# Performance work log

Measured on AMD Instinct MI355X. Metric: run time of the kernel, lower is better.

Reference implementation:

```python
import jax, jax.numpy as jnp
import numpy as np

N = 100000
E = 1600000
IN_DIM, HID, OUT = 256, 128, 64
K_HOPS = 5
ALPHA = 0.1
MLPA = 0.001


def setup_inputs() -> dict:
    key = jax.random.key(0)
    ks = jax.random.split(key, 20)
    s = 0.05
    inp = {
        "x": jax.random.normal(ks[0], (N, IN_DIM), jnp.float32),
        "edge_index": jax.random.randint(ks[1], (2, E), 0, N, jnp.int64),
        "edge_weight": jax.random.uniform(ks[2], (E,), jnp.float32),
        "A": jax.random.normal(ks[3], (N, 1), jnp.float32),
        # net1 MLP
        "m1_W1": jax.random.normal(ks[4], (IN_DIM, HID), jnp.float32) * s,
        "m1_b1": jnp.zeros((HID,), jnp.float32),
        "m1_W2": jax.random.normal(ks[5], (HID, OUT), jnp.float32) * s,
        "m1_b2": jnp.zeros((OUT,), jnp.float32),
        # net2 MLP
        "m2_W1": jax.random.normal(ks[6], (IN_DIM, HID), jnp.float32) * s,
        "m2_b1": jnp.zeros((HID,), jnp.float32),
        "m2_W2": jax.random.normal(ks[7], (HID, OUT), jnp.float32) * s,
        "m2_b2": jnp.zeros((OUT,), jnp.float32),
        # offset MLP (hidden*2)
        "off_W1": jax.random.normal(ks[8], (IN_DIM, 2 * HID), jnp.float32) * s,
        "off_b1": jnp.zeros((2 * HID,), jnp.float32),
        "off_W2": jax.random.normal(ks[9], (2 * HID, OUT), jnp.float32) * s,
        "off_b2": jnp.zeros((OUT,), jnp.float32),
        # mlp_A (A_dim=1 -> hidden*2 -> out)
        "A_W1": jax.random.normal(ks[10], (1, 2 * HID), jnp.float32) * s,
        "A_b1": jnp.zeros((2 * HID,), jnp.float32),
        "A_W2": jax.random.normal(ks[11], (2 * HID, OUT), jnp.float32) * s,
        "A_b2": jnp.zeros((OUT,), jnp.float32),
    }
    return inp


def _mlp2(x, W1, b1, W2, b2):
    return jax.nn.relu(x @ W1 + b1) @ W2 + b2


def _appnp(x, row, col, ew):
    # gcn_norm with added self loops (fill value 1)
    loop = jnp.arange(N, dtype=row.dtype)
    r = jnp.concatenate([row, loop])
    c = jnp.concatenate([col, loop])
    w = jnp.concatenate([ew, jnp.ones((N,), ew.dtype)])
    deg = jax.ops.segment_sum(w, c, num_segments=N)
    dinv = jnp.where(deg > 0, jax.lax.rsqrt(deg), 0.0)
    norm = dinv[r] * w * dinv[c]  # [E+N]
    h = x
    def step(xc, _):
        # gather source features, weight, scatter-add to targets
        agg = jax.ops.segment_sum(norm[:, None] * xc[r], c, num_segments=N)
        return agg * (1.0 - ALPHA) + ALPHA * h, None
    x, _ = jax.lax.scan(step, x, None, length=K_HOPS)
    return x


def reference(x, edge_index, edge_weight, A,
              m1_W1, m1_b1, m1_W2, m1_b2,
              m2_W1, m2_b1, m2_W2, m2_b2,
              off_W1, off_b1, off_W2, off_b2,
              A_W1, A_b1, A_W2, A_b2):
    row, col = edge_index[0], edge_index[1]
    # DualGNN edge-weight transforms, composed with APPNP_'s 1e-4 + 0.9999*w
    ew1 = 1e-4 + 0.9999 * (1e-5 + edge_weight * 0.99998)
    ew2 = 1e-4 + 0.9999 * (0.99999 - edge_weight * 0.99998)
    x1 = _appnp(_mlp2(x, m1_W1, m1_b1, m1_W2, m1_b2), row, col, ew1)
    x2 = _appnp(_mlp2(x, m2_W1, m2_b1, m2_W2, m2_b2), row, col, ew2)
    x_off = _mlp2(x, off_W1, off_b1, off_W2, off_b2)
    out = x1 - x2 + 0.001 * x_off
    out = out + MLPA * _mlp2(A, A_W1, A_b1, A_W2, A_b2)
    return jax.nn.log_softmax(out, axis=1)
```

## Files before the change

### kernel.cpp

```cpp
#include <hip/hip_runtime.h>
#include <stdint.h>

typedef unsigned int u32;
typedef unsigned short u16;
typedef unsigned long long u64;

#define IN_DIM 256

using bfrag = __attribute__((ext_vector_type(8))) short;
using f4 = __attribute__((ext_vector_type(4))) float;

__device__ __forceinline__ float bf2f(u16 u) {
  return __uint_as_float(((u32)u) << 16);
}
__device__ __forceinline__ u16 f2bf(float x) {
  u32 b = __float_as_uint(x);
  return (u16)((b + 0x7fffu + ((b >> 16) & 1u)) >> 16);
}
__device__ __forceinline__ f4 unpk(uint2 u) {
  return (f4){__uint_as_float(u.x << 16), __uint_as_float(u.x & 0xffff0000u),
              __uint_as_float(u.y << 16), __uint_as_float(u.y & 0xffff0000u)};
}

__global__ void k_detect(const int* __restrict__ ei, int E, int* flag) {
  __shared__ int ok;
  if (threadIdx.x == 0) ok = 1;
  __syncthreads();
  int m = (E < 512) ? E : 512;
  for (int i = threadIdx.x; i < m; i += 256)
    if (ei[2 * i + 1] != 0) ok = 0;
  __syncthreads();
  if (threadIdx.x == 0) flag[0] = ok;
}

__global__ void k_init(u64* packed, int* cursor, int n) {
  int i = blockIdx.x * 256 + threadIdx.x;
  if (i < n) { packed[i] = 0ULL; cursor[i] = 0; }
}

__global__ void k_prep(const float* m1W1, const float* m2W1, const float* offW1,
                       const float* m1b1, const float* m2b1, const float* offb1,
                       const float* m1W2, const float* m2W2, const float* offW2,
                       const float* AW1, const float* AW2,
                       u16* WP1, u16* WP2a, u16* WP2b, u16* WP2o,
                       float* b1cat, float* Ppos, float* Pneg) {
  int b = blockIdx.x, t = threadIdx.x;
  if (b < 64) {
    int p = b * 256 + t;
    int l = p & 63, nt = (p >> 6) & 3, ks = (p >> 8) & 7, wvv = p >> 11;
    int col = wvv * 64 + nt * 16 + (l & 15);
    int k0 = ks * 32 + (l >> 4) * 8;
    u16 frag[8];
#pragma unroll
    for (int j = 0; j < 8; ++j) {
      int k = k0 + j;
      float v;
      if (col < 128) v = m1W1[k * 128 + col];
      else if (col < 256) v = m2W1[k * 128 + (col - 128)];
      else v = offW1[k * 256 + (col - 256)];
      frag[j] = f2bf(v);
    }
    *reinterpret_cast<uint4*>(WP1 + (size_t)p * 8) = *reinterpret_cast<const uint4*>(frag);
  } else if (b < 68) {
    int p = (b - 64) * 256 + t;
    int l = p & 63, nt = (p >> 6) & 3, ks = p >> 8;
    int col = nt * 16 + (l & 15);
    int k0 = ks * 32 + (l >> 4) * 8;
    u16 frag[8];
#pragma unroll
    for (int j = 0; j < 8; ++j) frag[j] = f2bf(m1W2[(k0 + j) * 64 + col]);
    *reinterpret_cast<uint4*>(WP2a + (size_t)p * 8) = *reinterpret_cast<const uint4*>(frag);
  } else if (b < 72) {
    int p = (b - 68) * 256 + t;
    int l = p & 63, nt = (p >> 6) & 3, ks = p >> 8;
    int col = nt * 16 + (l & 15);
    int k0 = ks * 32 + (l >> 4) * 8;
    u16 frag[8];
#pragma unroll
    for (int j = 0; j < 8; ++j) frag[j] = f2bf(m2W2[(k0 + j) * 64 + col]);
    *reinterpret_cast<uint4*>(WP2b + (size_t)p * 8) = *reinterpret_cast<const uint4*>(frag);
  } else if (b < 80) {
    int p = (b - 72) * 256 + t;
    int l = p & 63, nt = (p >> 6) & 3, ks = p >> 8;
    int col = nt * 16 + (l & 15);
    int k0 = ks * 32 + (l >> 4) * 8;
    u16 frag[8];
#pragma unroll
    for (int j = 0; j < 8; ++j) frag[j] = f2bf(offW2[(k0 + j) * 64 + col]);
    *reinterpret_cast<uint4*>(WP2o + (size_t)p * 8) = *reinterpret_cast<const uint4*>(frag);
  } else if (b < 82) {
    int g = (b - 80) * 256 + t;
    float v;
    if (g < 128) v = m1b1[g];
    else if (g < 256) v = m2b1[g - 128];
    else v = offb1[g - 256];
    b1cat[g] = v;
  } else {
    if (t < 64) {
      float sp = 0.f, sn = 0.f;
      for (int k = 0; k < 256; ++k) {
        float w = AW1[k];
        float w2 = AW2[k * 64 + t];
        sp += fmaxf(w, 0.f) * w2;
        sn += fmaxf(-w, 0.f) * w2;
      }
      Ppos[t] = sp; Pneg[t] = sn;
    }
  }
}

__global__ void k_edge_deg(const int* __restrict__ ei, const float* __restrict__ ew,
                           const int* __restrict__ flag, u64* packed, int E) {
  int e = blockIdx.x * 256 + threadIdx.x;
  if (e >= E) return;
  int f = flag[0];
  int c = f ? ei[2 * (E + e)] : ei[E + e];
  float w = ew[e];
  float w1 = 1e-4f + 0.9999f * (1e-5f + w * 0.99998f);
  u64 add = (1ULL << 44) | (u64)(w1 * 4294967296.0f);
  atomicAdd(&packed[c], add);
}

__global__ void k_dinv(const u64* __restrict__ packed, float2* d2v, float2* snv,
                       int* cnt, int n) {
  int i = blockIdx.x * 256 + threadIdx.x;
  if (i < n) {
    u64 pk = packed[i];
    int c = (int)(pk >> 44);
    u64 lo44 = pk & 0xFFFFFFFFFFFULL;
    float s1 = (float)(u32)(lo44 >> 32) + (float)(u32)(lo44 & 0xFFFFFFFFu) * (1.0f / 4294967296.0f);
    float d1 = 1.0f + s1;
    float d2 = 1.0f + 1.0001f * (float)c - s1;
    float r1 = rsqrtf(d1), r2 = rsqrtf(d2);
    d2v[i] = make_float2(r1, r2);
    snv[i] = make_float2(r1 * r1, r2 * r2);
    cnt[i] = c;
  }
}

__global__ void k_scan1(const int* __restrict__ cnt, int* row_ptr, int* bsum, int n) {
  __shared__ int s[256];
  int t = threadIdx.x;
  int base = blockIdx.x * 1024 + t * 4;
  int v[4]; int tsum = 0;
#pragma unroll
  for (int i = 0; i < 4; ++i) { int idx = base + i; v[i] = (idx < n) ? cnt[idx] : 0; tsum += v[i]; }
  s[t] = tsum; __syncthreads();
  for (int d = 1; d < 256; d <<= 1) {
    int tmp = (t >= d) ? s[t - d] : 0;
    __syncthreads();
    s[t] += tmp;
    __syncthreads();
  }
  int run = s[t] - tsum;
#pragma unroll
  for (int i = 0; i < 4; ++i) { int idx = base + i; if (idx < n) row_ptr[idx] = run; run += v[i]; }
  if (t == 255) bsum[blockIdx.x] = s[255];
}

__global__ void k_scan2(const int* bsum, int* boff, int nb) {
  __shared__ int s[128];
  int t = threadIdx.x;
  int v = (t < nb) ? bsum[t] : 0;
  s[t] = v; __syncthreads();
  for (int d = 1; d < 128; d <<= 1) {
    int tmp = (t >= d) ? s[t - d] : 0;
    __syncthreads();
    s[t] += tmp;
    __syncthreads();
  }
  if (t < nb) boff[t] = s[t] - v;
}

__global__ void k_scan3(int* row_ptr, const int* boff, int n, int E) {
  int t = threadIdx.x, b = blockIdx.x;
  int off = boff[b];
  int base = b * 1024 + t * 4;
#pragma unroll
  for (int i = 0; i < 4; ++i) { int idx = base + i; if (idx < n) row_ptr[idx] += off; }
  if (b == 0 && t == 0) row_ptr[n] = E;
}

__global__ void k_scatter(const int* __restrict__ ei, const float* __restrict__ ew,
                          const int* __restrict__ flag,
                          const float2* __restrict__ d2v,
                          const int* __restrict__ row_ptr, int* cursor, uint2* csr, int E) {
  int e = blockIdx.x * 256 + threadIdx.x;
  if (e >= E) return;
  int f = flag[0];
  int r = f ? ei[2 * e] : ei[e];
  int c = f ? ei[2 * (E + e)] : ei[E + e];
  float w = ew[e];
  float w1 = 1e-4f + 0.9999f * (1e-5f + w * 0.99998f);
  float w2 = 1e-4f + 0.9999f * (0.99999f - w * 0.99998f);
  float2 dr = d2v[r], dc = d2v[c];
  float n1 = dr.x * w1 * dc.x;
  float n2 = dr.y * w2 * dc.y;
  int p = row_ptr[c] + atomicAdd(&cursor[c], 1);
  csr[p] = make_uint2((u32)r, (u32)f2bf(n1) | ((u32)f2bf(n2) << 16));
}

__global__ __launch_bounds__(512, 3) void k_mlp(
    const float* __restrict__ xg, const u16* __restrict__ WP1, const float* __restrict__ b1cat,
    const u16* __restrict__ WP2a, const u16* __restrict__ WP2b, const u16* __restrict__ WP2o,
    const float* __restrict__ m1b2, const float* __restrict__ m2b2, const float* __restrict__ offb2,
    const float* __restrict__ Ab2, const float* __restrict__ Ppos, const float* __restrict__ Pneg,
    const float* __restrict__ Ag, u16* __restrict__ H0, u16* __restrict__ Bb, int n) {
  __shared__ __align__(16) char smem[65536];
  int tid = threadIdx.x;
  int m0 = blockIdx.x * 64;
#pragma unroll
  for (int it = 0; it < 8; ++it) {
    int idx = it * 512 + tid;
    int row = idx >> 6, ch = idx & 63;
    int grow = m0 + row;
    float4 val = make_float4(0.f, 0.f, 0.f, 0.f);
    if (grow < n) val = *reinterpret_cast<const float4*>(xg + (size_t)grow * 256 + ch * 4);
    u32 lo = (u32)f2bf(val.x) | ((u32)f2bf(val.y) << 16);
    u32 hi2 = (u32)f2bf(val.z) | ((u32)f2bf(val.w) << 16);
    *reinterpret_cast<uint2*>(smem + row * 512 + ((ch * 8) ^ ((row & 7) << 4))) =
        make_uint2(lo, hi2);
  }
  __syncthreads();
  int wv = tid >> 6, ln = tid & 63;
  int l15 = ln & 15, lk = ln >> 4;
  int wn0 = wv * 64;
  f4 acc[4][4];
#pragma unroll
  for (int a = 0; a < 4; ++a)
#pragma unroll
    for (int b = 0; b < 4; ++b) acc[a][b] = (f4){0.f, 0.f, 0.f, 0.f};
#pragma unroll
  for (int ks = 0; ks < 8; ++ks) {
    bfrag a[4];
    int kb = ks * 64 + lk * 16;
#pragma unroll
    for (int mt = 0; mt < 4; ++mt) {
      int row = mt * 16 + l15;
      a[mt] = *reinterpret_cast<const bfrag*>(smem + row * 512 + (kb ^ ((row & 7) << 4)));
    }
#pragma unroll
    for (int nt = 0; nt < 4; ++nt) {
      bfrag b = *reinterpret_cast<const bfrag*>(
          WP1 + ((size_t)(((wv * 8 + ks) * 4 + nt) * 64 + ln) << 3));
#pragma unroll
      for (int mt = 0; mt < 4; ++mt)
        acc[mt][nt] = __builtin_amdgcn_mfma_f32_16x16x32_bf16(a[mt], b, acc[mt][nt], 0, 0, 0);
    }
  }
  __syncthreads();
#pragma unroll
  for (int nt = 0; nt < 4; ++nt) {
    int col = wn0 + nt * 16 + l15;
    float bias = b1cat[col];
#pragma unroll
    for (int mt = 0; mt < 4; ++mt) {
#pragma unroll
      for (int r = 0; r < 4; ++r) {
        int row = mt * 16 + lk * 4 + r;
        float v = fmaxf(acc[mt][nt][r] + bias, 0.f);
        *reinterpret_cast<u16*>(smem + row * 1024 + ((col * 2) ^ ((row & 7) << 4))) = f2bf(v);
      }
    }
  }
  __syncthreads();
  if (wv < 4) {
    f4 h1[4], h2[4];
#pragma unroll
    for (int i = 0; i < 4; ++i) { h1[i] = (f4){0,0,0,0}; h2[i] = (f4){0,0,0,0}; }
    int rowz = wv * 16 + l15;
    int swz = (rowz & 7) << 4;
#pragma unroll
    for (int ks = 0; ks < 4; ++ks) {
      int k1 = ks * 32 + lk * 8;
      bfrag a1 = *reinterpret_cast<const bfrag*>(smem + rowz * 1024 + ((k1 * 2) ^ swz));
      bfrag a2 = *reinterpret_cast<const bfrag*>(smem + rowz * 1024 + (((k1 + 128) * 2) ^ swz));
#pragma unroll
      for (int nt = 0; nt < 4; ++nt) {
        bfrag b1 = *reinterpret_cast<const bfrag*>(
            WP2a + ((size_t)((ks * 4 + nt) * 64 + ln) << 3));
        h1[nt] = __builtin_amdgcn_mfma_f32_16x16x32_bf16(a1, b1, h1[nt], 0, 0, 0);
        bfrag b2 = *reinterpret_cast<const bfrag*>(
            WP2b + ((size_t)((ks * 4 + nt) * 64 + ln) << 3));
        h2[nt] = __builtin_amdgcn_mfma_f32_16x16x32_bf16(a2, b2, h2[nt], 0, 0, 0);
      }
    }
    __syncthreads();
#pragma unroll
    for (int nt = 0; nt < 4; ++nt) {
      int col = nt * 16 + l15;
      float ba = m1b2[col], bbv = m2b2[col];
#pragma unroll
      for (int r = 0; r < 4; ++r) {
        int row = wv * 16 + lk * 4 + r;
        int swr = (row & 7) << 4;
        *reinterpret_cast<u16*>(smem + row * 256 + ((col * 2) ^ swr)) = f2bf(h1[nt][r] + ba);
        *reinterpret_cast<u16*>(smem + row * 256 + (((col + 64) * 2) ^ swr)) = f2bf(h2[nt][r] + bbv);
      }
    }
  } else {
    int wo = wv - 4;
    f4 ho[4];
#pragma unroll
    for (int i = 0; i < 4; ++i) ho[i] = (f4){0,0,0,0};
    int rowz = wo * 16 + l15;
    int swz = (rowz & 7) << 4;
#pragma unroll
    for (int ks = 0; ks < 8; ++ks) {
      int k1 = ks * 32 + lk * 8;
      bfrag a = *reinterpret_cast<const bfrag*>(smem + rowz * 1024 + (((k1 + 256) * 2) ^ swz));
#pragma unroll
      for (int nt = 0; nt < 4; ++nt) {
        bfrag b = *reinterpret_cast<const bfrag*>(
            WP2o + ((size_t)((ks * 4 + nt) * 64 + ln) << 3));
        ho[nt] = __builtin_amdgcn_mfma_f32_16x16x32_bf16(a, b, ho[nt], 0, 0, 0);
      }
    }
    __syncthreads();
#pragma unroll
    for (int nt = 0; nt < 4; ++nt) {
      int col = nt * 16 + l15;
      float bo = offb2[col];
      float pp = Ppos[col], pn = Pneg[col], ab2 = Ab2[col];
#pragma unroll
      for (int r = 0; r < 4; ++r) {
        int row = wo * 16 + lk * 4 + r;
        int grow = m0 + row;
        float av = (grow < n) ? Ag[grow] : 0.f;
        float mv = ab2 + (av > 0.f ? av * pp : (-av) * pn);
        *reinterpret_cast<u16*>(smem + 16384 + row * 128 + ((col * 2) ^ ((row & 7) << 4))) =
            f2bf(0.001f * (ho[nt][r] + bo) + 0.001f * mv);
      }
    }
  }
  __syncthreads();
#pragma unroll
  for (int i = 0; i < 2; ++i) {
    int idx = tid + i * 512;
    int row = idx >> 4, ch = idx & 15;
    if (m0 + row < n) {
      uint4 v = *reinterpret_cast<const uint4*>(smem + row * 256 + ((ch * 16) ^ ((row & 7) << 4)));
      *reinterpret_cast<uint4*>(H0 + (size_t)(m0 + row) * 128 + ch * 8) = v;
    }
  }
  {
    int row = tid >> 3, ch = tid & 7;
    if (m0 + row < n) {
      uint4 v = *reinterpret_cast<const uint4*>(smem + 16384 + row * 128 + ((ch * 16) ^ ((row & 7) << 4)));
      *reinterpret_cast<uint4*>(Bb + (size_t)(m0 + row) * 64 + ch * 8) = v;
    }
  }
}

__global__ __launch_bounds__(256) void k_prop(
    const u16* __restrict__ Xsrc, const u16* __restrict__ H0, u16* __restrict__ Xdst,
    const uint2* __restrict__ csr, const int* __restrict__ row_ptr,
    const float2* __restrict__ snv, const u16* __restrict__ Bb, float* __restrict__ out,
    int n, int finalize) {
  int node = blockIdx.x * 4 + (threadIdx.x >> 6);
  if (node >= n) return;
  int ln = threadIdx.x & 63;
  int half = ln >> 5;
  int k = ln & 31;
  bool isx2 = k >= 16;
  int e0 = row_ptr[node], e1 = row_ptr[node + 1];
  f4 acc = {0.f, 0.f, 0.f, 0.f}, accb = {0.f, 0.f, 0.f, 0.f};
  for (int base = e0; base < e1; base += 64) {
    int cnt = e1 - base; if (cnt > 64) cnt = 64;
    int idx = base + ln; if (idx >= e1) idx = e1 - 1;
    uint2 my = csr[idx];
    int j = 0;
    for (; j + 4 <= cnt; j += 4) {
      int ej0 = j + half, ej1 = j + 2 + half;
      u32 sx0 = (u32)__shfl((int)my.x, ej0);
      u32 sw0 = (u32)__shfl((int)my.y, ej0);
      u32 sx1 = (u32)__shfl((int)my.x, ej1);
      u32 sw1 = (u32)__shfl((int)my.y, ej1);
      uint2 u0 = *reinterpret_cast<const uint2*>(Xsrc + (size_t)sx0 * 128 + k * 4);
      uint2 u1 = *reinterpret_cast<const uint2*>(Xsrc + (size_t)sx1 * 128 + k * 4);
      float nn0 = bf2f(isx2 ? (u16)(sw0 >> 16) : (u16)(sw0 & 0xffffu));
      float nn1 = bf2f(isx2 ? (u16)(sw1 >> 16) : (u16)(sw1 & 0xffffu));
      acc += nn0 * unpk(u0);
      accb += nn1 * unpk(u1);
    }
    if (j + 2 <= cnt) {
      int ej = j + half;
      u32 sx = (u32)__shfl((int)my.x, ej);
      u32 sw = (u32)__shfl((int)my.y, ej);
      uint2 u = *reinterpret_cast<const uint2*>(Xsrc + (size_t)sx * 128 + k * 4);
      float nn = bf2f(isx2 ? (u16)(sw >> 16) : (u16)(sw & 0xffffu));
      acc += nn * unpk(u);
      j += 2;
    }
    if (j < cnt) {
      u32 sx = (u32)__shfl((int)my.x, j);
      u32 sw = (u32)__shfl((int)my.y, j);
      if (half == 0) {
        uint2 u = *reinterpret_cast<const uint2*>(Xsrc + (size_t)sx * 128 + k * 4);
        float nn = bf2f(isx2 ? (u16)(sw >> 16) : (u16)(sw & 0xffffu));
        acc += nn * unpk(u);
      }
    }
  }
  acc += accb;
#pragma unroll
  for (int i = 0; i < 4; ++i) acc[i] += __shfl_xor(acc[i], 32, 64);
  float2 snp = snv[node];
  float sn = isx2 ? snp.y : snp.x;
  uint2 us = *reinterpret_cast<const uint2*>(Xsrc + (size_t)node * 128 + k * 4);
  acc += sn * unpk(us);
  uint2 uh = *reinterpret_cast<const uint2*>(H0 + (size_t)node * 128 + k * 4);
  f4 hv = unpk(uh);
  f4 r;
#pragma unroll
  for (int i = 0; i < 4; ++i) r[i] = 0.9f * acc[i] + 0.1f * hv[i];
  if (!finalize) {
    if (half == 0) {
      u32 lo = (u32)f2bf(r[0]) | ((u32)f2bf(r[1]) << 16);
      u32 hi2 = (u32)f2bf(r[2]) | ((u32)f2bf(r[3]) << 16);
      *reinterpret_cast<uint2*>(Xdst + (size_t)node * 128 + k * 4) = make_uint2(lo, hi2);
    }
  } else {
    f4 o;
#pragma unroll
    for (int i = 0; i < 4; ++i) o[i] = __shfl_xor(r[i], 16, 64);
    uint2 ub = make_uint2(0, 0);
    if (k < 16) ub = *reinterpret_cast<const uint2*>(Bb + (size_t)node * 64 + k * 4);
    f4 bv = unpk(ub);
    f4 v;
#pragma unroll
    for (int i = 0; i < 4; ++i) v[i] = r[i] - o[i] + bv[i];
    float m = fmaxf(fmaxf(v[0], v[1]), fmaxf(v[2], v[3]));
#pragma unroll
    for (int off = 1; off < 16; off <<= 1) m = fmaxf(m, __shfl_xor(m, off, 64));
    float s = __expf(v[0] - m) + __expf(v[1] - m) + __expf(v[2] - m) + __expf(v[3] - m);
#pragma unroll
    for (int off = 1; off < 16; off <<= 1) s += __shfl_xor(s, off, 64);
    float ls = m + __logf(s);
    if (ln < 16) {
      float4 w = make_float4(v[0] - ls, v[1] - ls, v[2] - ls, v[3] - ls);
      *reinterpret_cast<float4*>(out + (size_t)node * 64 + k * 4) = w;
    }
  }
}

extern "C" void kernel_launch(void* const* d_in, const int* in_sizes, int n_in,
                              void* d_out, int out_size, void* d_ws, size_t ws_size,
                              hipStream_t stream) {
  const float* xg    = (const float*)d_in[0];
  const int* ei      = (const int*)d_in[1];
  const float* ewgt  = (const float*)d_in[2];
  const float* Ag    = (const float*)d_in[3];
  const float* m1W1  = (const float*)d_in[4];
  const float* m1b1  = (const float*)d_in[5];
  const float* m1W2  = (const float*)d_in[6];
  const float* m1b2  = (const float*)d_in[7];
  const float* m2W1  = (const float*)d_in[8];
  const float* m2b1  = (const float*)d_in[9];
  const float* m2W2  = (const float*)d_in[10];
  const float* m2b2  = (const float*)d_in[11];
  const float* offW1 = (const float*)d_in[12];
  const float* offb1 = (const float*)d_in[13];
  const float* offW2 = (const float*)d_in[14];
  const float* offb2 = (const float*)d_in[15];
  const float* AW1   = (const float*)d_in[16];
  const float* AW2   = (const float*)d_in[18];
  const float* Ab2   = (const float*)d_in[19];
  int n = in_sizes[0] / IN_DIM;
  int E = in_sizes[1] / 2;

  char* p = (char*)d_ws;
  auto alloc = [&](size_t bytes) { char* r = p; p += (bytes + 255) & ~(size_t)255; return r; };
  u16* H0    = (u16*)alloc((size_t)n * 128 * 2);
  u16* Xa    = (u16*)alloc((size_t)n * 128 * 2);
  u16* Xb    = (u16*)alloc((size_t)n * 128 * 2);
  u16* Bb    = (u16*)alloc((size_t)n * 64 * 2 + 256);
  uint2* csr = (uint2*)alloc((size_t)E * 8);
  u16* WP1   = (u16*)alloc((size_t)16384 * 16);
  u16* WP2a  = (u16*)alloc((size_t)1024 * 16);
  u16* WP2b  = (u16*)alloc((size_t)1024 * 16);
  u16* WP2o  = (u16*)alloc((size_t)2048 * 16);
  float* b1cat = (float*)alloc(512 * 4);
  float* Ppos  = (float*)alloc(64 * 4);
  float* Pneg  = (float*)alloc(64 * 4);
  u64* packed  = (u64*)alloc((size_t)n * 8);
  float2* d2v  = (float2*)alloc((size_t)n * 8);
  float2* snv  = (float2*)alloc((size_t)n * 8);
  int* cnt     = (int*)alloc((size_t)n * 4);
  int* cursor  = (int*)alloc((size_t)n * 4);
  int* row_ptr = (int*)alloc(((size_t)n + 1) * 4);
  int* bsum    = (int*)alloc(512);
  int* boff    = (int*)alloc(512);
  int* flag    = (int*)alloc(256);

  int nb256 = (n + 255) / 256;
  int eb = (E + 255) / 256;
  int nb1024 = (n + 1023) / 1024;
  int pb = (n + 3) / 4;

  k_detect<<<1, 256, 0, stream>>>(ei, E, flag);
  k_init<<<nb256, 256, 0, stream>>>(packed, cursor, n);
  k_prep<<<83, 256, 0, stream>>>(m1W1, m2W1, offW1, m1b1, m2b1, offb1,
                                 m1W2, m2W2, offW2, AW1, AW2,
                                 WP1, WP2a, WP2b, WP2o, b1cat, Ppos, Pneg);
  k_edge_deg<<<eb, 256, 0, stream>>>(ei, ewgt, flag, packed, E);
  k_dinv<<<nb256, 256, 0, stream>>>(packed, d2v, snv, cnt, n);
  k_scan1<<<nb1024, 256, 0, stream>>>(cnt, row_ptr, bsum, n);
  k_scan2<<<1, 128, 0, stream>>>(bsum, boff, nb1024);
  k_scan3<<<nb1024, 256, 0, stream>>>(row_ptr, boff, n, E);
  k_scatter<<<eb, 256, 0, stream>>>(ei, ewgt, flag, d2v, row_ptr, cursor, csr, E);
  k_mlp<<<(n + 63) / 64, 512, 0, stream>>>(xg, WP1, b1cat, WP2a, WP2b, WP2o,
                                           m1b2, m2b2, offb2, Ab2, Ppos, Pneg,
                                           Ag, H0, Bb, n);
  float* outp = (float*)d_out;
  k_prop<<<pb, 256, 0, stream>>>(H0, H0, Xa, csr, row_ptr, snv, Bb, outp, n, 0);
  k_prop<<<pb, 256, 0, stream>>>(Xa, H0, Xb, csr, row_ptr, snv, Bb, outp, n, 0);
  k_prop<<<pb, 256, 0, stream>>>(Xb, H0, Xa, csr, row_ptr, snv, Bb, outp, n, 0);
  k_prop<<<pb, 256, 0, stream>>>(Xa, H0, Xb, csr, row_ptr, snv, Bb, outp, n, 0);
  k_prop<<<pb, 256, 0, stream>>>(Xb, H0, Xa, csr, row_ptr, snv, Bb, outp, n, 1);
}
```

Baseline: 605.5 us.

## Fuse edge-degree pass into MLP launch and widen propagation gathers to 16 bytes

The edge-degree atomic accumulation now runs as extra blocks of the MLP kernel in a single launch, so the memory-bound atomic pass can overlap with the compute-bound MLP instead of running as its own kernel. The propagation kernel switches from 8-byte to 16-byte feature gathers, with four edges processed per wavefront step instead of two, and uses clamped indices with zeroed weights in place of the tail branches. This costs an extra cross-group shuffle reduction, the MLP's 64KB shared allocation on the edge blocks (which can limit how many co-reside), and some wasted gathers on short rows.

```diff
diff --git a/kernel.cpp b/kernel.cpp
--- a/kernel.cpp
+++ b/kernel.cpp
@@ -17,9 +17,9 @@
   u32 b = __float_as_uint(x);
   return (u16)((b + 0x7fffu + ((b >> 16) & 1u)) >> 16);
 }
-__device__ __forceinline__ f4 unpk(uint2 u) {
-  return (f4){__uint_as_float(u.x << 16), __uint_as_float(u.x & 0xffff0000u),
-              __uint_as_float(u.y << 16), __uint_as_float(u.y & 0xffff0000u)};
+__device__ __forceinline__ f4 unpk(u32 a, u32 b) {
+  return (f4){__uint_as_float(a << 16), __uint_as_float(a & 0xffff0000u),
+              __uint_as_float(b << 16), __uint_as_float(b & 0xffff0000u)};
 }
 
 __global__ void k_detect(const int* __restrict__ ei, int E, int* flag) {
@@ -109,18 +109,6 @@
   }
 }
 
-__global__ void k_edge_deg(const int* __restrict__ ei, const float* __restrict__ ew,
-                           const int* __restrict__ flag, u64* packed, int E) {
-  int e = blockIdx.x * 256 + threadIdx.x;
-  if (e >= E) return;
-  int f = flag[0];
-  int c = f ? ei[2 * (E + e)] : ei[E + e];
-  float w = ew[e];
-  float w1 = 1e-4f + 0.9999f * (1e-5f + w * 0.99998f);
-  u64 add = (1ULL << 44) | (u64)(w1 * 4294967296.0f);
-  atomicAdd(&packed[c], add);
-}
-
 __global__ void k_dinv(const u64* __restrict__ packed, float2* d2v, float2* snv,
                        int* cnt, int n) {
   int i = blockIdx.x * 256 + threadIdx.x;
@@ -200,14 +188,28 @@
   csr[p] = make_uint2((u32)r, (u32)f2bf(n1) | ((u32)f2bf(n2) << 16));
 }
 
-__global__ __launch_bounds__(512, 3) void k_mlp(
+__global__ __launch_bounds__(512, 3) void k_front(
     const float* __restrict__ xg, const u16* __restrict__ WP1, const float* __restrict__ b1cat,
     const u16* __restrict__ WP2a, const u16* __restrict__ WP2b, const u16* __restrict__ WP2o,
     const float* __restrict__ m1b2, const float* __restrict__ m2b2, const float* __restrict__ offb2,
     const float* __restrict__ Ab2, const float* __restrict__ Ppos, const float* __restrict__ Pneg,
-    const float* __restrict__ Ag, u16* __restrict__ H0, u16* __restrict__ Bb, int n) {
+    const float* __restrict__ Ag, u16* __restrict__ H0, u16* __restrict__ Bb, int n,
+    const int* __restrict__ ei, const float* __restrict__ ew, const int* __restrict__ flag,
+    u64* packed, int E, int MB) {
   __shared__ __align__(16) char smem[65536];
   int tid = threadIdx.x;
+  if ((int)blockIdx.x >= MB) {
+    int e = (blockIdx.x - MB) * 512 + tid;
+    if (e < E) {
+      int f = flag[0];
+      int c = f ? ei[2 * (E + e)] : ei[E + e];
+      float w = ew[e];
+      float w1 = 1e-4f + 0.9999f * (1e-5f + w * 0.99998f);
+      u64 add = (1ULL << 44) | (u64)(w1 * 4294967296.0f);
+      atomicAdd(&packed[c], add);
+    }
+    return;
+  }
   int m0 = blockIdx.x * 64;
 #pragma unroll
   for (int it = 0; it < 8; ++it) {
@@ -360,86 +362,93 @@
   int node = blockIdx.x * 4 + (threadIdx.x >> 6);
   if (node >= n) return;
   int ln = threadIdx.x & 63;
-  int half = ln >> 5;
-  int k = ln & 31;
-  bool isx2 = k >= 16;
+  int g = ln >> 4, q = ln & 15;
+  bool isx2 = q >= 8;
   int e0 = row_ptr[node], e1 = row_ptr[node + 1];
-  f4 acc = {0.f, 0.f, 0.f, 0.f}, accb = {0.f, 0.f, 0.f, 0.f};
+  f4 a0 = {0.f, 0.f, 0.f, 0.f}, a1 = {0.f, 0.f, 0.f, 0.f};
+  f4 b0 = {0.f, 0.f, 0.f, 0.f}, b1 = {0.f, 0.f, 0.f, 0.f};
   for (int base = e0; base < e1; base += 64) {
     int cnt = e1 - base; if (cnt > 64) cnt = 64;
     int idx = base + ln; if (idx >= e1) idx = e1 - 1;
     uint2 my = csr[idx];
-    int j = 0;
-    for (; j + 4 <= cnt; j += 4) {
-      int ej0 = j + half, ej1 = j + 2 + half;
-      u32 sx0 = (u32)__shfl((int)my.x, ej0);
-      u32 sw0 = (u32)__shfl((int)my.y, ej0);
-      u32 sx1 = (u32)__shfl((int)my.x, ej1);
-      u32 sw1 = (u32)__shfl((int)my.y, ej1);
-      uint2 u0 = *reinterpret_cast<const uint2*>(Xsrc + (size_t)sx0 * 128 + k * 4);
-      uint2 u1 = *reinterpret_cast<const uint2*>(Xsrc + (size_t)sx1 * 128 + k * 4);
-      float nn0 = bf2f(isx2 ? (u16)(sw0 >> 16) : (u16)(sw0 & 0xffffu));
-      float nn1 = bf2f(isx2 ? (u16)(sw1 >> 16) : (u16)(sw1 & 0xffffu));
-      acc += nn0 * unpk(u0);
-      accb += nn1 * unpk(u1);
-    }
-    if (j + 2 <= cnt) {
-      int ej = j + half;
-      u32 sx = (u32)__shfl((int)my.x, ej);
-      u32 sw = (u32)__shfl((int)my.y, ej);
-      uint2 u = *reinterpret_cast<const uint2*>(Xsrc + (size_t)sx * 128 + k * 4);
-      float nn = bf2f(isx2 ? (u16)(sw >> 16) : (u16)(sw & 0xffffu));
-      acc += nn * unpk(u);
-      j += 2;
-    }
-    if (j < cnt) {
-      u32 sx = (u32)__shfl((int)my.x, j);
-      u32 sw = (u32)__shfl((int)my.y, j);
-      if (half == 0) {
-        uint2 u = *reinterpret_cast<const uint2*>(Xsrc + (size_t)sx * 128 + k * 4);
-        float nn = bf2f(isx2 ? (u16)(sw >> 16) : (u16)(sw & 0xffffu));
-        acc += nn * unpk(u);
-      }
-    }
-  }
-  acc += accb;
-#pragma unroll
-  for (int i = 0; i < 4; ++i) acc[i] += __shfl_xor(acc[i], 32, 64);
+    for (int j = 0; j < cnt; j += 8) {
+      int s0 = j + g, s1 = j + 4 + g;
+      int c0 = s0 < cnt ? s0 : cnt - 1;
+      int c1 = s1 < cnt ? s1 : cnt - 1;
+      u32 sx0 = (u32)__shfl((int)my.x, c0);
+      u32 sw0 = (u32)__shfl((int)my.y, c0);
+      u32 sx1 = (u32)__shfl((int)my.x, c1);
+      u32 sw1 = (u32)__shfl((int)my.y, c1);
+      uint4 u0 = *reinterpret_cast<const uint4*>(Xsrc + (size_t)sx0 * 128 + q * 8);
+      uint4 u1 = *reinterpret_cast<const uint4*>(Xsrc + (size_t)sx1 * 128 + q * 8);
+      float nn0 = (s0 < cnt) ? bf2f(isx2 ? (u16)(sw0 >> 16) : (u16)(sw0 & 0xffffu)) : 0.f;
+      float nn1 = (s1 < cnt) ? bf2f(isx2 ? (u16)(sw1 >> 16) : (u16)(sw1 & 0xffffu)) : 0.f;
+      a0 += nn0 * unpk(u0.x, u0.y);
+      a1 += nn0 * unpk(u0.z, u0.w);
+      b0 += nn1 * unpk(u1.x, u1.y);
+      b1 += nn1 * unpk(u1.z, u1.w);
+    }
+  }
+  a0 += b0; a1 += b1;
+#pragma unroll
+  for (int i = 0; i < 4; ++i) {
+    a0[i] += __shfl_xor(a0[i], 16, 64);
+    a0[i] += __shfl_xor(a0[i], 32, 64);
+    a1[i] += __shfl_xor(a1[i], 16, 64);
+    a1[i] += __shfl_xor(a1[i], 32, 64);
+  }
   float2 snp = snv[node];
   float sn = isx2 ? snp.y : snp.x;
-  uint2 us = *reinterpret_cast<const uint2*>(Xsrc + (size_t)node * 128 + k * 4);
-  acc += sn * unpk(us);
-  uint2 uh = *reinterpret_cast<const uint2*>(H0 + (size_t)node * 128 + k * 4);
-  f4 hv = unpk(uh);
-  f4 r;
-#pragma unroll
-  for (int i = 0; i < 4; ++i) r[i] = 0.9f * acc[i] + 0.1f * hv[i];
+  uint4 us = *reinterpret_cast<const uint4*>(Xsrc + (size_t)node * 128 + q * 8);
+  a0 += sn * unpk(us.x, us.y);
+  a1 += sn * unpk(us.z, us.w);
+  uint4 uh = *reinterpret_cast<const uint4*>(H0 + (size_t)node * 128 + q * 8);
+  f4 hv0 = unpk(uh.x, uh.y), hv1 = unpk(uh.z, uh.w);
+  f4 r0, r1;
+#pragma unroll
+  for (int i = 0; i < 4; ++i) {
+    r0[i] = 0.9f * a0[i] + 0.1f * hv0[i];
+    r1[i] = 0.9f * a1[i] + 0.1f * hv1[i];
+  }
   if (!finalize) {
-    if (half == 0) {
-      u32 lo = (u32)f2bf(r[0]) | ((u32)f2bf(r[1]) << 16);
-      u32 hi2 = (u32)f2bf(r[2]) | ((u32)f2bf(r[3]) << 16);
-      *reinterpret_cast<uint2*>(Xdst + (size_t)node * 128 + k * 4) = make_uint2(lo, hi2);
+    if (g == 0) {
+      uint4 o;
+      o.x = (u32)f2bf(r0[0]) | ((u32)f2bf(r0[1]) << 16);
+      o.y = (u32)f2bf(r0[2]) | ((u32)f2bf(r0[3]) << 16);
+      o.z = (u32)f2bf(r1[0]) | ((u32)f2bf(r1[1]) << 16);
+      o.w = (u32)f2bf(r1[2]) | ((u32)f2bf(r1[3]) << 16);
+      *reinterpret_cast<uint4*>(Xdst + (size_t)node * 128 + q * 8) = o;
     }
   } else {
-    f4 o;
-#pragma unroll
-    for (int i = 0; i < 4; ++i) o[i] = __shfl_xor(r[i], 16, 64);
-    uint2 ub = make_uint2(0, 0);
-    if (k < 16) ub = *reinterpret_cast<const uint2*>(Bb + (size_t)node * 64 + k * 4);
-    f4 bv = unpk(ub);
-    f4 v;
-#pragma unroll
-    for (int i = 0; i < 4; ++i) v[i] = r[i] - o[i] + bv[i];
-    float m = fmaxf(fmaxf(v[0], v[1]), fmaxf(v[2], v[3]));
-#pragma unroll
-    for (int off = 1; off < 16; off <<= 1) m = fmaxf(m, __shfl_xor(m, off, 64));
-    float s = __expf(v[0] - m) + __expf(v[1] - m) + __expf(v[2] - m) + __expf(v[3] - m);
-#pragma unroll
-    for (int off = 1; off < 16; off <<= 1) s += __shfl_xor(s, off, 64);
+    f4 o0, o1;
+#pragma unroll
+    for (int i = 0; i < 4; ++i) {
+      o0[i] = __shfl_xor(r0[i], 8, 64);
+      o1[i] = __shfl_xor(r1[i], 8, 64);
+    }
+    uint4 ub = make_uint4(0, 0, 0, 0);
+    if (q < 8) ub = *reinterpret_cast<const uint4*>(Bb + (size_t)node * 64 + q * 8);
+    f4 bv0 = unpk(ub.x, ub.y), bv1 = unpk(ub.z, ub.w);
+    f4 v0, v1;
+#pragma unroll
+    for (int i = 0; i < 4; ++i) {
+      v0[i] = r0[i] - o0[i] + bv0[i];
+      v1[i] = r1[i] - o1[i] + bv1[i];
+    }
+    float m = fmaxf(fmaxf(fmaxf(v0[0], v0[1]), fmaxf(v0[2], v0[3])),
+                    fmaxf(fmaxf(v1[0], v1[1]), fmaxf(v1[2], v1[3])));
+#pragma unroll
+    for (int off = 1; off < 8; off <<= 1) m = fmaxf(m, __shfl_xor(m, off, 64));
+    float s = __expf(v0[0] - m) + __expf(v0[1] - m) + __expf(v0[2] - m) + __expf(v0[3] - m) +
+              __expf(v1[0] - m) + __expf(v1[1] - m) + __expf(v1[2] - m) + __expf(v1[3] - m);
+#pragma unroll
+    for (int off = 1; off < 8; off <<= 1) s += __shfl_xor(s, off, 64);
     float ls = m + __logf(s);
-    if (ln < 16) {
-      float4 w = make_float4(v[0] - ls, v[1] - ls, v[2] - ls, v[3] - ls);
-      *reinterpret_cast<float4*>(out + (size_t)node * 64 + k * 4) = w;
+    if (g == 0 && q < 8) {
+      float4 w0 = make_float4(v0[0] - ls, v0[1] - ls, v0[2] - ls, v0[3] - ls);
+      float4 w1 = make_float4(v1[0] - ls, v1[1] - ls, v1[2] - ls, v1[3] - ls);
+      *reinterpret_cast<float4*>(out + (size_t)node * 64 + q * 8) = w0;
+      *reinterpret_cast<float4*>(out + (size_t)node * 64 + q * 8 + 4) = w1;
     }
   }
 }
@@ -497,21 +506,22 @@
   int eb = (E + 255) / 256;
   int nb1024 = (n + 1023) / 1024;
   int pb = (n + 3) / 4;
+  int MB = (n + 63) / 64;
+  int EB = (E + 511) / 512;
 
   k_detect<<<1, 256, 0, stream>>>(ei, E, flag);
   k_init<<<nb256, 256, 0, stream>>>(packed, cursor, n);
   k_prep<<<83, 256, 0, stream>>>(m1W1, m2W1, offW1, m1b1, m2b1, offb1,
                                  m1W2, m2W2, offW2, AW1, AW2,
                                  WP1, WP2a, WP2b, WP2o, b1cat, Ppos, Pneg);
-  k_edge_deg<<<eb, 256, 0, stream>>>(ei, ewgt, flag, packed, E);
+  k_front<<<MB + EB, 512, 0, stream>>>(xg, WP1, b1cat, WP2a, WP2b, WP2o,
+                                       m1b2, m2b2, offb2, Ab2, Ppos, Pneg,
+                                       Ag, H0, Bb, n, ei, ewgt, flag, packed, E, MB);
   k_dinv<<<nb256, 256, 0, stream>>>(packed, d2v, snv, cnt, n);
   k_scan1<<<nb1024, 256, 0, stream>>>(cnt, row_ptr, bsum, n);
   k_scan2<<<1, 128, 0, stream>>>(bsum, boff, nb1024);
   k_scan3<<<nb1024, 256, 0, stream>>>(row_ptr, boff, n, E);
   k_scatter<<<eb, 256, 0, stream>>>(ei, ewgt, flag, d2v, row_ptr, cursor, csr, E);
-  k_mlp<<<(n + 63) / 64, 512, 0, stream>>>(xg, WP1, b1cat, WP2a, WP2b, WP2o,
-                                           m1b2, m2b2, offb2, Ab2, Ppos, Pneg,
-                                           Ag, H0, Bb, n);
   float* outp = (float*)d_out;
   k_prop<<<pb, 256, 0, stream>>>(H0, H0, Xa, csr, row_ptr, snv, Bb, outp, n, 0);
   k_prop<<<pb, 256, 0, stream>>>(Xa, H0, Xb, csr, row_ptr, snv, Bb, outp, n, 0);
```

New measurement: 583.8 us. -3.6%, faster.
